# Kernel tuning notes

Hardware: AMD Instinct MI355X
Metric: run time of the kernel (lower is better)

Reference implementation:

```python
import jax, jax.numpy as jnp
import numpy as np

N_NODES = 50000
N_EDGES = 800000
N_LABEL = 200000
IN_C, HID_C, OUT_C = 128, 128, 64


def setup_inputs() -> dict:
    key = jax.random.key(0)
    ks = jax.random.split(key, 9)
    s = lambda fan_in: 1.0 / np.sqrt(fan_in)
    return {
        "x": jax.random.normal(ks[0], (N_NODES, IN_C), jnp.float32),
        "W1": jax.random.normal(ks[1], (IN_C, HID_C), jnp.float32) * s(IN_C),
        "b1": jnp.zeros((HID_C,), jnp.float32),
        "W2": jax.random.normal(ks[2], (HID_C, HID_C), jnp.float32) * s(HID_C),
        "b2": jnp.zeros((HID_C,), jnp.float32),
        "W3": jax.random.normal(ks[3], (HID_C, OUT_C), jnp.float32) * s(HID_C),
        "b3": jnp.zeros((OUT_C,), jnp.float32),
        "edge_index": jax.random.randint(ks[4], (2, N_EDGES), 0, N_NODES, jnp.int32),
        "edge_label_index": jax.random.randint(ks[5], (2, N_LABEL), 0, N_NODES, jnp.int32),
    }


def _gcn_conv(x, W, b, src, dst, dinv, num_nodes):
    # x @ W then symmetric-normalized scatter-sum over edges (self-loops included in src/dst)
    h = x @ W                                  # [N, out]
    norm = dinv[src] * dinv[dst]               # [E+N]
    msgs = h[src] * norm[:, None]              # [E+N, out]
    out = jax.ops.segment_sum(msgs, dst, num_segments=num_nodes)
    return out + b


def _encode(x, W1, b1, W2, b2, W3, b3, edge_index, num_nodes):
    loops = jnp.arange(num_nodes, dtype=edge_index.dtype)
    src = jnp.concatenate([edge_index[0], loops])
    dst = jnp.concatenate([edge_index[1], loops])
    # degree (with self-loops) at targets; deg >= 1 so rsqrt is safe
    deg = jax.ops.segment_sum(jnp.ones(dst.shape[0], x.dtype), dst, num_segments=num_nodes)
    dinv = jax.lax.rsqrt(deg)
    z = _gcn_conv(x, W1, b1, src, dst, dinv, num_nodes)
    z = jax.nn.relu(z)  # dropout treated as eval-mode identity
    z = _gcn_conv(z, W2, b2, src, dst, dinv, num_nodes)
    z = jax.nn.relu(z)
    z = _gcn_conv(z, W3, b3, src, dst, dinv, num_nodes)
    return z


def reference(x, W1, b1, W2, b2, W3, b3, edge_index, edge_label_index):
    z = _encode(x, W1, b1, W2, b2, W3, b3, edge_index, N_NODES)
    # decode: gather both endpoints, elementwise mul, sum over feature dim
    return (z[edge_label_index[0]] * z[edge_label_index[1]]).sum(axis=-1)
```

## Files before the change

kernel.cpp:

```cpp
#include <hip/hip_runtime.h>

#define N_NODES 50000
#define N_EDGES 800000
#define N_LABEL 200000
#define ROW_BLOCKS 782

typedef __attribute__((ext_vector_type(4))) float f32x4;
typedef _Float16 f16;
typedef __attribute__((ext_vector_type(8))) _Float16 f16x8;


__global__ __launch_bounds__(256)
void k_zero(int4* __restrict__ p, int n4) {
    int i = blockIdx.x * 256 + threadIdx.x;
    if (i < n4) p[i] = int4{0, 0, 0, 0};
}

__global__ __launch_bounds__(256)
void k_prep(const float* __restrict__ W1, const float* __restrict__ W2,
            const float* __restrict__ W3,
            f16* WT1h, f16* WT1l, f16* WT2h, f16* WT2l, f16* WT3h, f16* WT3l,
            const int* __restrict__ dst, int* cnt) {
    int b = blockIdx.x, tid = threadIdx.x;
    if (b < 64) {
        int t = b * 256 + tid;
        int c = t >> 7, k = t & 127;
        float w = W1[k * 128 + c];
        f16 h = (f16)w;
        WT1h[c * 128 + k] = h; WT1l[c * 128 + k] = (f16)(w - (float)h);
        w = W2[k * 128 + c];
        h = (f16)w;
        WT2h[c * 128 + k] = h; WT2l[c * 128 + k] = (f16)(w - (float)h);
        if (c < 64) {
            w = W3[k * 64 + c];
            h = (f16)w;
            WT3h[c * 128 + k] = h; WT3l[c * 128 + k] = (f16)(w - (float)h);
        }
    } else {
        int vb = b - 64;
        int g = vb & 7;
        int i = (vb >> 3) * 256 + tid;
        int d = dst[i];
        if ((unsigned)(d - g * 6250) < 6250u) atomicAdd(&cnt[d], 1);
    }
}

__global__ __launch_bounds__(256)
void k_partial(const int* __restrict__ cnt, float* __restrict__ dinv,
               int* __restrict__ bsum, int N) {
    __shared__ int wsum[4];
    int b = blockIdx.x, t = threadIdx.x;
    int i = b * 256 + t;
    int v = (i < N) ? cnt[i] : 0;
    if (i < N) dinv[i] = rsqrtf((float)v + 1.0f);
    int s = v;
#pragma unroll
    for (int d = 1; d < 64; d <<= 1) s += __shfl_xor(s, d, 64);
    if ((t & 63) == 0) wsum[t >> 6] = s;
    __syncthreads();
    if (t == 0) bsum[b] = wsum[0] + wsum[1] + wsum[2] + wsum[3];
}

__global__ __launch_bounds__(256)
void k_offsets(const int* __restrict__ cnt, const int* __restrict__ bsum,
               int* __restrict__ off, int N, int NB) {
    __shared__ int wsum[4];
    __shared__ int add0_s;
    int b = blockIdx.x, t = threadIdx.x;
    int v0 = (t < b && t < NB) ? bsum[t] : 0;
    int s0 = v0;
#pragma unroll
    for (int d = 1; d < 64; d <<= 1) s0 += __shfl_xor(s0, d, 64);
    if ((t & 63) == 0) wsum[t >> 6] = s0;
    __syncthreads();
    if (t == 0) add0_s = wsum[0] + wsum[1] + wsum[2] + wsum[3];
    __syncthreads();
    int add = add0_s;
    __syncthreads();
    int i = b * 256 + t;
    int v = (i < N) ? cnt[i] : 0;
    int lane = t & 63, w = t >> 6;
    int sv = v;
#pragma unroll
    for (int d = 1; d < 64; d <<= 1) {
        int u = __shfl_up(sv, d, 64);
        if (lane >= d) sv += u;
    }
    if (lane == 63) wsum[w] = sv;
    __syncthreads();
    for (int ww = 0; ww < w; ++ww) add += wsum[ww];
    if (i < N) off[i + 1] = add + sv;
    if (i == 0) off[0] = 0;
}

__global__ __launch_bounds__(256)
void k_bucket(const int* __restrict__ srcv, const int* __restrict__ dstv,
              const int* __restrict__ off, int* cnt2, unsigned short* __restrict__ csr) {
    int vb = blockIdx.x;
    int g = vb & 7;
    int i = (vb >> 3) * 256 + threadIdx.x;
    int d = dstv[i];
    if ((unsigned)(d - g * 6250) < 6250u) {
        int slot = off[d] + atomicAdd(&cnt2[d], 1);
        csr[slot] = (unsigned short)srcv[i];
    }
}

__global__ __launch_bounds__(256)
void k_gemm1(const float* __restrict__ x,
             const f16* __restrict__ WTh, const f16* __restrict__ WTl,
             const float* __restrict__ dinv, f16* __restrict__ As, int N) {
    constexpr int NCB = 4;
    __shared__ f16 Hs[64 * 136];
    __shared__ f16 Ls[64 * 136];
    int b = blockIdx.x;
    int c0 = (b & 1) * 64;
    int t = threadIdx.x;

#pragma unroll
    for (int i = 0; i < 4; ++i) {
        int ch = t + i * 256;
        int col = ch >> 4;
        int kc = (ch & 15) * 8;
        *(f16x8*)&Hs[col * 136 + kc] = *(const f16x8*)&WTh[(long)(c0 + col) * 128 + kc];
        *(f16x8*)&Ls[col * 136 + kc] = *(const f16x8*)&WTl[(long)(c0 + col) * 128 + kc];
    }

    int wv = t >> 6, l = t & 63;
    int r0w = (b >> 1) * 64 + wv * 16;
    int arow = r0w + (l & 15);
    if (arow >= N) arow = N - 1;
    int kb = (l >> 4) * 8;

    f16x8 ah[4], al[4];
#pragma unroll
    for (int ks = 0; ks < 4; ++ks) {
        const float* xp = &x[(long)arow * 128 + ks * 32 + kb];
        float4 a0 = *(const float4*)xp;
        float4 a1 = *(const float4*)(xp + 4);
        float fv[8] = {a0.x, a0.y, a0.z, a0.w, a1.x, a1.y, a1.z, a1.w};
#pragma unroll
        for (int j = 0; j < 8; ++j) {
            f16 h = (f16)fv[j];
            ah[ks][j] = h;
            al[ks][j] = (f16)(fv[j] - (float)h);
        }
    }
    __syncthreads();

    f32x4 acc[NCB];
#pragma unroll
    for (int cb = 0; cb < NCB; ++cb) acc[cb] = f32x4{0.f, 0.f, 0.f, 0.f};
#pragma unroll
    for (int ks = 0; ks < 4; ++ks) {
#pragma unroll
        for (int cb = 0; cb < NCB; ++cb) {
            int wi = (cb * 16 + (l & 15)) * 136 + ks * 32 + kb;
            f16x8 bh = *(const f16x8*)&Hs[wi];
            f16x8 bl = *(const f16x8*)&Ls[wi];
            acc[cb] = __builtin_amdgcn_mfma_f32_16x16x32_f16(ah[ks], bh, acc[cb], 0, 0, 0);
            acc[cb] = __builtin_amdgcn_mfma_f32_16x16x32_f16(ah[ks], bl, acc[cb], 0, 0, 0);
            acc[cb] = __builtin_amdgcn_mfma_f32_16x16x32_f16(al[ks], bh, acc[cb], 0, 0, 0);
        }
    }
    int rbase = r0w + (l >> 4) * 4;
    float dv[4];
#pragma unroll
    for (int i = 0; i < 4; ++i) dv[i] = (rbase + i < N) ? dinv[rbase + i] : 0.f;
#pragma unroll
    for (int cb = 0; cb < NCB; ++cb) {
        int fc = c0 + cb * 16 + (l & 15);
        long sb = (long)(fc >> 5) * N_NODES * 32 + (fc & 31);
#pragma unroll
        for (int i = 0; i < 4; ++i) {
            int r = rbase + i;
            if (r < N) As[sb + (long)r * 32] = (f16)(acc[cb][i] * dv[i]);
        }
    }
}

template<int M>
__global__ __launch_bounds__(256)
void k_gemm23(const f16* __restrict__ Bs,
              const f16* __restrict__ WTh, const f16* __restrict__ WTl,
              const float* __restrict__ dinv, f16* __restrict__ As, int N) {
    constexpr int NCB = M / 32;
    constexpr int HC = M / 2;
    __shared__ f16 Hs[HC * 136];
    __shared__ f16 Ls[HC * 136];
    int b = blockIdx.x;
    int c0 = (b & 1) * HC;
    int t = threadIdx.x;

#pragma unroll
    for (int i = 0; i < HC / 16; ++i) {
        int ch = t + i * 256;
        int col = ch >> 4;
        int kc = (ch & 15) * 8;
        *(f16x8*)&Hs[col * 136 + kc] = *(const f16x8*)&WTh[(long)(c0 + col) * 128 + kc];
        *(f16x8*)&Ls[col * 136 + kc] = *(const f16x8*)&WTl[(long)(c0 + col) * 128 + kc];
    }

    int wv = t >> 6, l = t & 63;
    int r0w = (b >> 1) * 64 + wv * 16;
    int arow = r0w + (l & 15);
    if (arow >= N) arow = N - 1;
    int kb = (l >> 4) * 8;

    f16x8 a[4];
#pragma unroll
    for (int ks = 0; ks < 4; ++ks)
        a[ks] = *(const f16x8*)&Bs[((long)ks * N_NODES + arow) * 32 + kb];
    __syncthreads();

    f32x4 acc[NCB];
#pragma unroll
    for (int cb = 0; cb < NCB; ++cb) acc[cb] = f32x4{0.f, 0.f, 0.f, 0.f};
#pragma unroll
    for (int ks = 0; ks < 4; ++ks) {
#pragma unroll
        for (int cb = 0; cb < NCB; ++cb) {
            int wi = (cb * 16 + (l & 15)) * 136 + ks * 32 + kb;
            f16x8 bh = *(const f16x8*)&Hs[wi];
            f16x8 bl = *(const f16x8*)&Ls[wi];
            acc[cb] = __builtin_amdgcn_mfma_f32_16x16x32_f16(a[ks], bh, acc[cb], 0, 0, 0);
            acc[cb] = __builtin_amdgcn_mfma_f32_16x16x32_f16(a[ks], bl, acc[cb], 0, 0, 0);
        }
    }
    int rbase = r0w + (l >> 4) * 4;
    float dv[4];
#pragma unroll
    for (int i = 0; i < 4; ++i) dv[i] = (rbase + i < N) ? dinv[rbase + i] : 0.f;
#pragma unroll
    for (int cb = 0; cb < NCB; ++cb) {
        int fc = c0 + cb * 16 + (l & 15);
        long sb = (long)(fc >> 5) * N_NODES * 32 + (fc & 31);
#pragma unroll
        for (int i = 0; i < 4; ++i) {
            int r = rbase + i;
            if (r < N) As[sb + (long)r * 32] = (f16)(acc[cb][i] * dv[i]);
        }
    }
}

__global__ __launch_bounds__(256)
void k_gather128(const f16* __restrict__ As, const int* __restrict__ off,
                 const unsigned short* __restrict__ csr, const float* __restrict__ dinv,
                 const float* __restrict__ bias, f16* __restrict__ Bs) {
    int vb = blockIdx.x;
    int g = vb & 7, blk = vb >> 3;
    int t = threadIdx.x;
    int nl = blk * 64 + (t >> 2);
    if (nl >= 25000) return;
    int node = (g & 1) * 25000 + nl;
    int cs = g >> 1;
    int qq = (t & 3) * 8;
    const f16* Aq = As + (long)cs * N_NODES * 32 + qq;

    float acc[8];
    {
        f16x8 v = *(const f16x8*)&Aq[(long)node * 32];
#pragma unroll
        for (int c = 0; c < 8; ++c) acc[c] = (float)v[c];
    }
    int j = off[node], j1 = off[node + 1];
    for (; j + 8 <= j1; j += 8) {
        int s0 = csr[j + 0], s1 = csr[j + 1], s2 = csr[j + 2], s3 = csr[j + 3];
        int s4 = csr[j + 4], s5 = csr[j + 5], s6 = csr[j + 6], s7 = csr[j + 7];
        f16x8 v0 = *(const f16x8*)&Aq[(long)s0 * 32];
        f16x8 v1 = *(const f16x8*)&Aq[(long)s1 * 32];
        f16x8 v2 = *(const f16x8*)&Aq[(long)s2 * 32];
        f16x8 v3 = *(const f16x8*)&Aq[(long)s3 * 32];
        f16x8 v4 = *(const f16x8*)&Aq[(long)s4 * 32];
        f16x8 v5 = *(const f16x8*)&Aq[(long)s5 * 32];
        f16x8 v6 = *(const f16x8*)&Aq[(long)s6 * 32];
        f16x8 v7 = *(const f16x8*)&Aq[(long)s7 * 32];
#pragma unroll
        for (int c = 0; c < 8; ++c)
            acc[c] += ((float)v0[c] + (float)v1[c] + (float)v2[c] + (float)v3[c])
                    + ((float)v4[c] + (float)v5[c] + (float)v6[c] + (float)v7[c]);
    }
    for (; j + 2 <= j1; j += 2) {
        int s0 = csr[j + 0], s1 = csr[j + 1];
        f16x8 v0 = *(const f16x8*)&Aq[(long)s0 * 32];
        f16x8 v1 = *(const f16x8*)&Aq[(long)s1 * 32];
#pragma unroll
        for (int c = 0; c < 8; ++c) acc[c] += (float)v0[c] + (float)v1[c];
    }
    if (j < j1) {
        int s = csr[j];
        f16x8 v = *(const f16x8*)&Aq[(long)s * 32];
#pragma unroll
        for (int c = 0; c < 8; ++c) acc[c] += (float)v[c];
    }
    float sc = dinv[node];
    int q = cs * 32 + qq;
    float4 bb0 = *(const float4*)&bias[q];
    float4 bb1 = *(const float4*)&bias[q + 4];
    float bv[8] = {bb0.x, bb0.y, bb0.z, bb0.w, bb1.x, bb1.y, bb1.z, bb1.w};
    f16x8 o;
#pragma unroll
    for (int c = 0; c < 8; ++c) o[c] = (f16)fmaxf(acc[c] * sc + bv[c], 0.f);
    *(f16x8*)&Bs[((long)cs * N_NODES + node) * 32 + qq] = o;
}

__global__ __launch_bounds__(256)
void k_gather64(const f16* __restrict__ As, const int* __restrict__ off,
                const unsigned short* __restrict__ csr, const float* __restrict__ dinv,
                const float* __restrict__ bias, float* __restrict__ z) {
    int vb = blockIdx.x;
    int g = vb & 7, blk = vb >> 3;
    int t = threadIdx.x;
    int nl = blk * 64 + (t >> 2);
    if (nl >= 12500) return;
    int node = (g >> 1) * 12500 + nl;
    int cs = g & 1;
    int qq = (t & 3) * 8;
    const f16* Aq = As + (long)cs * N_NODES * 32 + qq;

    float acc[8];
    {
        f16x8 v = *(const f16x8*)&Aq[(long)node * 32];
#pragma unroll
        for (int c = 0; c < 8; ++c) acc[c] = (float)v[c];
    }
    int j = off[node], j1 = off[node + 1];
    for (; j + 8 <= j1; j += 8) {
        int s0 = csr[j + 0], s1 = csr[j + 1], s2 = csr[j + 2], s3 = csr[j + 3];
        int s4 = csr[j + 4], s5 = csr[j + 5], s6 = csr[j + 6], s7 = csr[j + 7];
        f16x8 v0 = *(const f16x8*)&Aq[(long)s0 * 32];
        f16x8 v1 = *(const f16x8*)&Aq[(long)s1 * 32];
        f16x8 v2 = *(const f16x8*)&Aq[(long)s2 * 32];
        f16x8 v3 = *(const f16x8*)&Aq[(long)s3 * 32];
        f16x8 v4 = *(const f16x8*)&Aq[(long)s4 * 32];
        f16x8 v5 = *(const f16x8*)&Aq[(long)s5 * 32];
        f16x8 v6 = *(const f16x8*)&Aq[(long)s6 * 32];
        f16x8 v7 = *(const f16x8*)&Aq[(long)s7 * 32];
#pragma unroll
        for (int c = 0; c < 8; ++c)
            acc[c] += ((float)v0[c] + (float)v1[c] + (float)v2[c] + (float)v3[c])
                    + ((float)v4[c] + (float)v5[c] + (float)v6[c] + (float)v7[c]);
    }
    for (; j + 2 <= j1; j += 2) {
        int s0 = csr[j + 0], s1 = csr[j + 1];
        f16x8 v0 = *(const f16x8*)&Aq[(long)s0 * 32];
        f16x8 v1 = *(const f16x8*)&Aq[(long)s1 * 32];
#pragma unroll
        for (int c = 0; c < 8; ++c) acc[c] += (float)v0[c] + (float)v1[c];
    }
    if (j < j1) {
        int s = csr[j];
        f16x8 v = *(const f16x8*)&Aq[(long)s * 32];
#pragma unroll
        for (int c = 0; c < 8; ++c) acc[c] += (float)v[c];
    }
    float sc = dinv[node];
    int q = cs * 32 + qq;
    float4 bb0 = *(const float4*)&bias[q];
    float4 bb1 = *(const float4*)&bias[q + 4];
    float4 o0, o1;
    o0.x = acc[0] * sc + bb0.x; o0.y = acc[1] * sc + bb0.y;
    o0.z = acc[2] * sc + bb0.z; o0.w = acc[3] * sc + bb0.w;
    o1.x = acc[4] * sc + bb1.x; o1.y = acc[5] * sc + bb1.y;
    o1.z = acc[6] * sc + bb1.z; o1.w = acc[7] * sc + bb1.w;
    *(float4*)&z[(long)node * 64 + q] = o0;
    *(float4*)&z[(long)node * 64 + q + 4] = o1;
}

__global__ void k_decode(const float* __restrict__ z, const int* __restrict__ eli,
                         float* __restrict__ out, int L) {
    int t = blockIdx.x * blockDim.x + threadIdx.x;
    int e = t >> 4;
    int lane = t & 15;
    if (e >= L) return;
    int a = eli[e], b = eli[L + e];
    float4 va = *(const float4*)&z[(long)a * 64 + lane * 4];
    float4 vb = *(const float4*)&z[(long)b * 64 + lane * 4];
    float s = va.x * vb.x + va.y * vb.y + va.z * vb.z + va.w * vb.w;
    s += __shfl_xor(s, 1, 16);
    s += __shfl_xor(s, 2, 16);
    s += __shfl_xor(s, 4, 16);
    s += __shfl_xor(s, 8, 16);
    if (lane == 0) out[e] = s;
}

extern "C" void kernel_launch(void* const* d_in, const int* in_sizes, int n_in,
                              void* d_out, int out_size, void* d_ws, size_t ws_size,
                              hipStream_t stream) {
    const float* x   = (const float*)d_in[0];
    const float* W1  = (const float*)d_in[1];
    const float* b1  = (const float*)d_in[2];
    const float* W2  = (const float*)d_in[3];
    const float* b2  = (const float*)d_in[4];
    const float* W3  = (const float*)d_in[5];
    const float* b3  = (const float*)d_in[6];
    const int*   ei  = (const int*)d_in[7];
    const int*   eli = (const int*)d_in[8];
    float* out = (float*)d_out;

    char* ws = (char*)d_ws;
    float* dinv = (float*)ws;                  ws += 50048 * 4;
    f16*   A    = (f16*)ws;                    ws += (long)N_NODES * 128 * 2;
    f16*   B    = (f16*)ws;                    ws += (long)N_NODES * 128 * 2;
    float* z    = (float*)ws;                  ws += (long)N_NODES * 64 * 4;
    int*   cnt  = (int*)ws;                    ws += 50048 * 4;
    int*   cnt2 = (int*)ws;                    ws += 50048 * 4;
    int*   off  = (int*)ws;                    ws += 50048 * 4;
    unsigned short* csr = (unsigned short*)ws; ws += (long)N_EDGES * 2;
    int*   bsum = (int*)ws;                    ws += 256 * 4;
    f16*   WT1h = (f16*)ws;                    ws += 16384 * 2;
    f16*   WT1l = (f16*)ws;                    ws += 16384 * 2;
    f16*   WT2h = (f16*)ws;                    ws += 16384 * 2;
    f16*   WT2l = (f16*)ws;                    ws += 16384 * 2;
    f16*   WT3h = (f16*)ws;                    ws += 8192 * 2;
    f16*   WT3l = (f16*)ws;                    ws += 8192 * 2;

    const int* esrc = ei;
    const int* edst = ei + N_EDGES;

    const int NB = (N_NODES + 255) / 256;

    k_zero   <<<98, 256, 0, stream>>>((int4*)cnt, 25024);
    k_prep   <<<25064, 256, 0, stream>>>(W1, W2, W3, WT1h, WT1l, WT2h, WT2l,
                                         WT3h, WT3l, edst, cnt);
    k_partial<<<NB, 256, 0, stream>>>(cnt, dinv, bsum, N_NODES);
    k_offsets<<<NB, 256, 0, stream>>>(cnt, bsum, off, N_NODES, NB);
    k_bucket <<<25000, 256, 0, stream>>>(esrc, edst, off, cnt2, csr);

    k_gemm1<<<ROW_BLOCKS * 2, 256, 0, stream>>>(x, WT1h, WT1l, dinv, A, N_NODES);
    k_gather128<<<391 * 8, 256, 0, stream>>>(A, off, csr, dinv, b1, B);
    k_gemm23<128><<<ROW_BLOCKS * 2, 256, 0, stream>>>(B, WT2h, WT2l, dinv, A, N_NODES);
    k_gather128<<<391 * 8, 256, 0, stream>>>(A, off, csr, dinv, b2, B);
    k_gemm23<64><<<ROW_BLOCKS * 2, 256, 0, stream>>>(B, WT3h, WT3l, dinv, A, N_NODES);
    k_gather64<<<196 * 8, 256, 0, stream>>>(A, off, csr, dinv, b3, z);

    k_decode<<<(N_LABEL * 16 + 255) / 256, 256, 0, stream>>>(z, eli, out, N_LABEL);
}
```

Measured before the change: 209.8 us.

## Compact edge indices to 16-bit and split decode into column-sliced partial sums

```diff
diff --git a/kernel.cpp b/kernel.cpp
--- a/kernel.cpp
+++ b/kernel.cpp
@@ -11,16 +11,25 @@
 
 
 __global__ __launch_bounds__(256)
-void k_zero(int4* __restrict__ p, int n4) {
-    int i = blockIdx.x * 256 + threadIdx.x;
-    if (i < n4) p[i] = int4{0, 0, 0, 0};
+void k_zero(int4* __restrict__ p, const int* __restrict__ esrc,
+            const int* __restrict__ edst, unsigned short* __restrict__ src16,
+            unsigned short* __restrict__ dst16) {
+    int b = blockIdx.x, tid = threadIdx.x;
+    if (b < 98) {
+        int i = b * 256 + tid;
+        if (i < 25024) p[i] = int4{0, 0, 0, 0};
+    } else {
+        int i = (b - 98) * 256 + tid;
+        src16[i] = (unsigned short)esrc[i];
+        dst16[i] = (unsigned short)edst[i];
+    }
 }
 
 __global__ __launch_bounds__(256)
 void k_prep(const float* __restrict__ W1, const float* __restrict__ W2,
             const float* __restrict__ W3,
             f16* WT1h, f16* WT1l, f16* WT2h, f16* WT2l, f16* WT3h, f16* WT3l,
-            const int* __restrict__ dst, int* cnt) {
+            const unsigned short* __restrict__ dst16, int* cnt) {
     int b = blockIdx.x, tid = threadIdx.x;
     if (b < 64) {
         int t = b * 256 + tid;
@@ -40,7 +49,7 @@
         int vb = b - 64;
         int g = vb & 7;
         int i = (vb >> 3) * 256 + tid;
-        int d = dst[i];
+        int d = dst16[i];
         if ((unsigned)(d - g * 6250) < 6250u) atomicAdd(&cnt[d], 1);
     }
 }
@@ -94,15 +103,16 @@
 }
 
 __global__ __launch_bounds__(256)
-void k_bucket(const int* __restrict__ srcv, const int* __restrict__ dstv,
+void k_bucket(const unsigned short* __restrict__ src16,
+              const unsigned short* __restrict__ dst16,
               const int* __restrict__ off, int* cnt2, unsigned short* __restrict__ csr) {
     int vb = blockIdx.x;
     int g = vb & 7;
     int i = (vb >> 3) * 256 + threadIdx.x;
-    int d = dstv[i];
+    int d = dst16[i];
     if ((unsigned)(d - g * 6250) < 6250u) {
         int slot = off[d] + atomicAdd(&cnt2[d], 1);
-        csr[slot] = (unsigned short)srcv[i];
+        csr[slot] = src16[i];
     }
 }
 
@@ -307,7 +317,7 @@
 __global__ __launch_bounds__(256)
 void k_gather64(const f16* __restrict__ As, const int* __restrict__ off,
                 const unsigned short* __restrict__ csr, const float* __restrict__ dinv,
-                const float* __restrict__ bias, float* __restrict__ z) {
+                const float* __restrict__ bias, float* __restrict__ zs) {
     int vb = blockIdx.x;
     int g = vb & 7, blk = vb >> 3;
     int t = threadIdx.x;
@@ -363,25 +373,38 @@
     o0.z = acc[2] * sc + bb0.z; o0.w = acc[3] * sc + bb0.w;
     o1.x = acc[4] * sc + bb1.x; o1.y = acc[5] * sc + bb1.y;
     o1.z = acc[6] * sc + bb1.z; o1.w = acc[7] * sc + bb1.w;
-    *(float4*)&z[(long)node * 64 + q] = o0;
-    *(float4*)&z[(long)node * 64 + q + 4] = o1;
-}
-
-__global__ void k_decode(const float* __restrict__ z, const int* __restrict__ eli,
-                         float* __restrict__ out, int L) {
-    int t = blockIdx.x * blockDim.x + threadIdx.x;
-    int e = t >> 4;
-    int lane = t & 15;
-    if (e >= L) return;
-    int a = eli[e], b = eli[L + e];
-    float4 va = *(const float4*)&z[(long)a * 64 + lane * 4];
-    float4 vb = *(const float4*)&z[(long)b * 64 + lane * 4];
-    float s = va.x * vb.x + va.y * vb.y + va.z * vb.z + va.w * vb.w;
-    s += __shfl_xor(s, 1, 16);
-    s += __shfl_xor(s, 2, 16);
-    s += __shfl_xor(s, 4, 16);
-    s += __shfl_xor(s, 8, 16);
-    if (lane == 0) out[e] = s;
+    long zb = (long)(q >> 4) * N_NODES * 16 + (long)node * 16 + (q & 15);
+    *(float4*)&zs[zb] = o0;
+    *(float4*)&zs[zb + 4] = o1;
+}
+
+__global__ __launch_bounds__(256)
+void k_decode_part(const float* __restrict__ zs, const int* __restrict__ eli,
+                   float* __restrict__ P) {
+    int vb = blockIdx.x;
+    int g = vb & 7, blk = vb >> 3;
+    int el = blk * 256 + threadIdx.x;
+    if (el >= 100000) return;
+    int e = (g & 1) * 100000 + el;
+    int cs = g >> 1;
+    const float* zsl = zs + (long)cs * N_NODES * 16;
+    const float* za = &zsl[(long)eli[e] * 16];
+    const float* zb = &zsl[(long)eli[N_LABEL + e] * 16];
+    float s = 0.f;
+#pragma unroll
+    for (int i = 0; i < 4; ++i) {
+        float4 a = *(const float4*)&za[i * 4];
+        float4 b = *(const float4*)&zb[i * 4];
+        s += a.x * b.x + a.y * b.y + a.z * b.z + a.w * b.w;
+    }
+    P[cs * N_LABEL + e] = s;
+}
+
+__global__ __launch_bounds__(256)
+void k_decode_red(const float* __restrict__ P, float* __restrict__ out) {
+    int e = blockIdx.x * 256 + threadIdx.x;
+    if (e < N_LABEL)
+        out[e] = (P[e] + P[N_LABEL + e]) + (P[2 * N_LABEL + e] + P[3 * N_LABEL + e]);
 }
 
 extern "C" void kernel_launch(void* const* d_in, const int* in_sizes, int n_in,
@@ -402,11 +425,14 @@
     float* dinv = (float*)ws;                  ws += 50048 * 4;
     f16*   A    = (f16*)ws;                    ws += (long)N_NODES * 128 * 2;
     f16*   B    = (f16*)ws;                    ws += (long)N_NODES * 128 * 2;
-    float* z    = (float*)ws;                  ws += (long)N_NODES * 64 * 4;
+    float* zs   = (float*)ws;                  ws += (long)N_NODES * 64 * 4;
+    float* P    = (float*)ws;                  ws += (long)4 * N_LABEL * 4;
     int*   cnt  = (int*)ws;                    ws += 50048 * 4;
     int*   cnt2 = (int*)ws;                    ws += 50048 * 4;
     int*   off  = (int*)ws;                    ws += 50048 * 4;
-    unsigned short* csr = (unsigned short*)ws; ws += (long)N_EDGES * 2;
+    unsigned short* csr   = (unsigned short*)ws; ws += (long)N_EDGES * 2;
+    unsigned short* src16 = (unsigned short*)ws; ws += (long)N_EDGES * 2;
+    unsigned short* dst16 = (unsigned short*)ws; ws += (long)N_EDGES * 2;
     int*   bsum = (int*)ws;                    ws += 256 * 4;
     f16*   WT1h = (f16*)ws;                    ws += 16384 * 2;
     f16*   WT1l = (f16*)ws;                    ws += 16384 * 2;
@@ -420,19 +446,20 @@
 
     const int NB = (N_NODES + 255) / 256;
 
-    k_zero   <<<98, 256, 0, stream>>>((int4*)cnt, 25024);
+    k_zero   <<<98 + 3125, 256, 0, stream>>>((int4*)cnt, esrc, edst, src16, dst16);
     k_prep   <<<25064, 256, 0, stream>>>(W1, W2, W3, WT1h, WT1l, WT2h, WT2l,
-                                         WT3h, WT3l, edst, cnt);
+                                         WT3h, WT3l, dst16, cnt);
     k_partial<<<NB, 256, 0, stream>>>(cnt, dinv, bsum, N_NODES);
     k_offsets<<<NB, 256, 0, stream>>>(cnt, bsum, off, N_NODES, NB);
-    k_bucket <<<25000, 256, 0, stream>>>(esrc, edst, off, cnt2, csr);
+    k_bucket <<<25000, 256, 0, stream>>>(src16, dst16, off, cnt2, csr);
 
     k_gemm1<<<ROW_BLOCKS * 2, 256, 0, stream>>>(x, WT1h, WT1l, dinv, A, N_NODES);
     k_gather128<<<391 * 8, 256, 0, stream>>>(A, off, csr, dinv, b1, B);
     k_gemm23<128><<<ROW_BLOCKS * 2, 256, 0, stream>>>(B, WT2h, WT2l, dinv, A, N_NODES);
     k_gather128<<<391 * 8, 256, 0, stream>>>(A, off, csr, dinv, b2, B);
     k_gemm23<64><<<ROW_BLOCKS * 2, 256, 0, stream>>>(B, WT3h, WT3l, dinv, A, N_NODES);
-    k_gather64<<<196 * 8, 256, 0, stream>>>(A, off, csr, dinv, b3, z);
-
-    k_decode<<<(N_LABEL * 16 + 255) / 256, 256, 0, stream>>>(z, eli, out, N_LABEL);
-}
+    k_gather64<<<196 * 8, 256, 0, stream>>>(A, off, csr, dinv, b3, zs);
+
+    k_decode_part<<<391 * 8, 256, 0, stream>>>(zs, eli, P);
+    k_decode_red <<<(N_LABEL + 255) / 256, 256, 0, stream>>>(P, out);
+}
```

After: 216.0 us. +3.0%, slower.

## Compress edge indices to 16-bit and merge preprocessing kernels

Applied to the files above, without the earlier changes.

```diff
diff --git a/kernel.cpp b/kernel.cpp
--- a/kernel.cpp
+++ b/kernel.cpp
@@ -11,19 +11,18 @@
 
 
 __global__ __launch_bounds__(256)
-void k_zero(int4* __restrict__ p, int n4) {
-    int i = blockIdx.x * 256 + threadIdx.x;
-    if (i < n4) p[i] = int4{0, 0, 0, 0};
-}
-
-__global__ __launch_bounds__(256)
-void k_prep(const float* __restrict__ W1, const float* __restrict__ W2,
-            const float* __restrict__ W3,
-            f16* WT1h, f16* WT1l, f16* WT2h, f16* WT2l, f16* WT3h, f16* WT3l,
-            const int* __restrict__ dst, int* cnt) {
+void k_pre(int4* __restrict__ p,
+           const float* __restrict__ W1, const float* __restrict__ W2,
+           const float* __restrict__ W3,
+           f16* WT1h, f16* WT1l, f16* WT2h, f16* WT2l, f16* WT3h, f16* WT3l,
+           const int* __restrict__ esrc, const int* __restrict__ edst,
+           unsigned short* __restrict__ src16, unsigned short* __restrict__ dst16) {
     int b = blockIdx.x, tid = threadIdx.x;
-    if (b < 64) {
-        int t = b * 256 + tid;
+    if (b < 98) {
+        int i = b * 256 + tid;
+        if (i < 25024) p[i] = int4{0, 0, 0, 0};
+    } else if (b < 162) {
+        int t = (b - 98) * 256 + tid;
         int c = t >> 7, k = t & 127;
         float w = W1[k * 128 + c];
         f16 h = (f16)w;
@@ -37,48 +36,40 @@
             WT3h[c * 128 + k] = h; WT3l[c * 128 + k] = (f16)(w - (float)h);
         }
     } else {
-        int vb = b - 64;
-        int g = vb & 7;
-        int i = (vb >> 3) * 256 + tid;
-        int d = dst[i];
-        if ((unsigned)(d - g * 6250) < 6250u) atomicAdd(&cnt[d], 1);
-    }
-}
-
-__global__ __launch_bounds__(256)
-void k_partial(const int* __restrict__ cnt, float* __restrict__ dinv,
-               int* __restrict__ bsum, int N) {
+        int i = (b - 162) * 256 + tid;
+        src16[i] = (unsigned short)esrc[i];
+        dst16[i] = (unsigned short)edst[i];
+    }
+}
+
+__global__ __launch_bounds__(256)
+void k_deg(const unsigned short* __restrict__ dst16, int* cnt) {
+    int vb = blockIdx.x;
+    int g = vb & 7;
+    int i = (vb >> 3) * 256 + threadIdx.x;
+    int d = dst16[i];
+    if ((unsigned)(d - g * 6250) < 6250u) atomicAdd(&cnt[d], 1);
+}
+
+__global__ __launch_bounds__(256)
+void k_offs(const int* __restrict__ cnt, float* __restrict__ dinv,
+            int* __restrict__ off, int N) {
     __shared__ int wsum[4];
+    __shared__ int add0_s;
     int b = blockIdx.x, t = threadIdx.x;
+    int s = 0;
+    for (int k = t; k < b * 256; k += 256) s += cnt[k];
+#pragma unroll
+    for (int d = 1; d < 64; d <<= 1) s += __shfl_xor(s, d, 64);
+    if ((t & 63) == 0) wsum[t >> 6] = s;
+    __syncthreads();
+    if (t == 0) add0_s = wsum[0] + wsum[1] + wsum[2] + wsum[3];
+    __syncthreads();
+    int add = add0_s;
+    __syncthreads();
     int i = b * 256 + t;
     int v = (i < N) ? cnt[i] : 0;
     if (i < N) dinv[i] = rsqrtf((float)v + 1.0f);
-    int s = v;
-#pragma unroll
-    for (int d = 1; d < 64; d <<= 1) s += __shfl_xor(s, d, 64);
-    if ((t & 63) == 0) wsum[t >> 6] = s;
-    __syncthreads();
-    if (t == 0) bsum[b] = wsum[0] + wsum[1] + wsum[2] + wsum[3];
-}
-
-__global__ __launch_bounds__(256)
-void k_offsets(const int* __restrict__ cnt, const int* __restrict__ bsum,
-               int* __restrict__ off, int N, int NB) {
-    __shared__ int wsum[4];
-    __shared__ int add0_s;
-    int b = blockIdx.x, t = threadIdx.x;
-    int v0 = (t < b && t < NB) ? bsum[t] : 0;
-    int s0 = v0;
-#pragma unroll
-    for (int d = 1; d < 64; d <<= 1) s0 += __shfl_xor(s0, d, 64);
-    if ((t & 63) == 0) wsum[t >> 6] = s0;
-    __syncthreads();
-    if (t == 0) add0_s = wsum[0] + wsum[1] + wsum[2] + wsum[3];
-    __syncthreads();
-    int add = add0_s;
-    __syncthreads();
-    int i = b * 256 + t;
-    int v = (i < N) ? cnt[i] : 0;
     int lane = t & 63, w = t >> 6;
     int sv = v;
 #pragma unroll
@@ -94,15 +85,16 @@
 }
 
 __global__ __launch_bounds__(256)
-void k_bucket(const int* __restrict__ srcv, const int* __restrict__ dstv,
+void k_bucket(const unsigned short* __restrict__ src16,
+              const unsigned short* __restrict__ dst16,
               const int* __restrict__ off, int* cnt2, unsigned short* __restrict__ csr) {
     int vb = blockIdx.x;
     int g = vb & 7;
     int i = (vb >> 3) * 256 + threadIdx.x;
-    int d = dstv[i];
+    int d = dst16[i];
     if ((unsigned)(d - g * 6250) < 6250u) {
         int slot = off[d] + atomicAdd(&cnt2[d], 1);
-        csr[slot] = (unsigned short)srcv[i];
+        csr[slot] = src16[i];
     }
 }
 
@@ -406,8 +398,9 @@
     int*   cnt  = (int*)ws;                    ws += 50048 * 4;
     int*   cnt2 = (int*)ws;                    ws += 50048 * 4;
     int*   off  = (int*)ws;                    ws += 50048 * 4;
-    unsigned short* csr = (unsigned short*)ws; ws += (long)N_EDGES * 2;
-    int*   bsum = (int*)ws;                    ws += 256 * 4;
+    unsigned short* csr   = (unsigned short*)ws; ws += (long)N_EDGES * 2;
+    unsigned short* src16 = (unsigned short*)ws; ws += (long)N_EDGES * 2;
+    unsigned short* dst16 = (unsigned short*)ws; ws += (long)N_EDGES * 2;
     f16*   WT1h = (f16*)ws;                    ws += 16384 * 2;
     f16*   WT1l = (f16*)ws;                    ws += 16384 * 2;
     f16*   WT2h = (f16*)ws;                    ws += 16384 * 2;
@@ -420,12 +413,12 @@
 
     const int NB = (N_NODES + 255) / 256;
 
-    k_zero   <<<98, 256, 0, stream>>>((int4*)cnt, 25024);
-    k_prep   <<<25064, 256, 0, stream>>>(W1, W2, W3, WT1h, WT1l, WT2h, WT2l,
-                                         WT3h, WT3l, edst, cnt);
-    k_partial<<<NB, 256, 0, stream>>>(cnt, dinv, bsum, N_NODES);
-    k_offsets<<<NB, 256, 0, stream>>>(cnt, bsum, off, N_NODES, NB);
-    k_bucket <<<25000, 256, 0, stream>>>(esrc, edst, off, cnt2, csr);
+    k_pre   <<<3287, 256, 0, stream>>>((int4*)cnt, W1, W2, W3,
+                                       WT1h, WT1l, WT2h, WT2l, WT3h, WT3l,
+                                       esrc, edst, src16, dst16);
+    k_deg   <<<25000, 256, 0, stream>>>(dst16, cnt);
+    k_offs  <<<NB, 256, 0, stream>>>(cnt, dinv, off, N_NODES);
+    k_bucket<<<25000, 256, 0, stream>>>(src16, dst16, off, cnt2, csr);
 
     k_gemm1<<<ROW_BLOCKS * 2, 256, 0, stream>>>(x, WT1h, WT1l, dinv, A, N_NODES);
     k_gather128<<<391 * 8, 256, 0, stream>>>(A, off, csr, dinv, b1, B);
```

Result: slower. 233.1 us (+11.1%).
